# Optimization experiments

Measured on AMD Instinct MI355X. Metric: run time of the kernel, lower is better.

## Reference

```python
import jax, jax.numpy as jnp
import numpy as np

WS = 7
NUM_HEADS = 4


def setup_inputs() -> dict:
    key = jax.random.key(0)
    ks = jax.random.split(key, 5)
    C = 128
    return {
        "x": jax.random.normal(ks[0], (8, 222, 222, C), dtype=jnp.float32),
        "qkv_w": jax.random.normal(ks[1], (C, 3 * C), dtype=jnp.float32) * 0.02,
        "qkv_b": jax.random.normal(ks[2], (3 * C,), dtype=jnp.float32) * 0.02,
        "proj_w": jax.random.normal(ks[3], (C, C), dtype=jnp.float32) * 0.02,
        "proj_b": jax.random.normal(ks[4], (C,), dtype=jnp.float32) * 0.02,
    }


def reference(x, qkv_w, qkv_b, proj_w, proj_b):
    B, H, W, C = x.shape
    ws, nh = WS, NUM_HEADS
    hd = C // nh
    scale = hd ** (-0.5)
    pad_h = (ws - H % ws) % ws
    pad_w = (ws - W % ws) % ws
    xp = jnp.pad(x, ((0, 0), (0, pad_h), (0, pad_w), (0, 0)))
    Hp, Wp = H + pad_h, W + pad_w
    # window partition: [B,Hp,Wp,C] -> [nW, ws*ws, C]
    xw = xp.reshape(B, Hp // ws, ws, Wp // ws, ws, C)
    xw = xw.transpose(0, 1, 3, 2, 4, 5).reshape(-1, ws * ws, C)
    # qkv projection
    qkv = xw @ qkv_w + qkv_b  # [nW, 49, 3C]
    qkv = qkv.reshape(-1, ws * ws, 3, nh, hd).transpose(2, 0, 3, 1, 4)
    q, k, v = qkv[0], qkv[1], qkv[2]  # each [nW, nh, 49, hd]
    attn = jax.nn.softmax(jnp.einsum('whqd,whkd->whqk', q, k) * scale, axis=-1)
    out = jnp.einsum('whqk,whkd->whqd', attn, v)  # [nW, nh, 49, hd]
    out = out.transpose(0, 2, 1, 3).reshape(-1, ws * ws, C)
    out = out @ proj_w + proj_b
    # window reverse: [nW, ws*ws, C] -> [B, Hp, Wp, C]
    out = out.reshape(B, Hp // ws, Wp // ws, ws, ws, C)
    out = out.transpose(0, 1, 3, 2, 4, 5).reshape(B, Hp, Wp, C)
    return out[:, :H, :W, :]
```

## Files before the change

### kernel.cpp

```cpp
#include <hip/hip_runtime.h>
#include <stdint.h>

typedef __attribute__((ext_vector_type(8))) short bf16x8;
typedef __attribute__((ext_vector_type(4))) float f32x4;
typedef __attribute__((ext_vector_type(4))) unsigned int u32x4;

#define IMG 222

__device__ __forceinline__ unsigned short f2bf(float f){
  unsigned int u = __float_as_uint(f);
  return (unsigned short)((u + 0x7fffu + ((u >> 16) & 1u)) >> 16);
}

__device__ __forceinline__ unsigned int pk2bf(float lo, float hi){
  unsigned int r;
  asm("v_cvt_pk_bf16_f32 %0, %1, %2" : "=v"(r) : "v"(lo), "v"(hi));
  return r;
}

__device__ __forceinline__ int sw128(int r, int c){ return r*128 + (c ^ ((r & 7) << 3)); }
__device__ __forceinline__ int sw64 (int r, int c){ return r*64  + (c ^ ((r & 7) << 3)); }

__global__ void prep_weights(const float* __restrict__ qkv_w,
                             const float* __restrict__ proj_w,
                             unsigned short* __restrict__ qwt,
                             unsigned short* __restrict__ pwt){
  int i = blockIdx.x * blockDim.x + threadIdx.x;
  if (i < 384*128){ int n = i >> 7, k = i & 127; qwt[i] = f2bf(qkv_w[k*384 + n]); }
  if (i < 128*128){ int n = i >> 7, k = i & 127; pwt[i] = f2bf(proj_w[k*128 + n]); }
}

__global__ __launch_bounds__(256, 4)
void win_attn(const float* __restrict__ x,
              const float* __restrict__ qkv_b,
              const float* __restrict__ proj_b,
              const unsigned short* __restrict__ qwt,
              const unsigned short* __restrict__ pwt,
              float* __restrict__ out)
{
  extern __shared__ unsigned short lds[];
  unsigned short* r0 = lds;
  unsigned short* r1 = lds + 8192;
  unsigned short* r2 = lds + 16384;

  const int tid = threadIdx.x;
  const int wid = tid >> 6;
  const int l   = tid & 63;
  const int l15 = l & 15;
  const int lhi = l >> 4;

  const int w  = (blockIdx.x & 7) * 1024 + (blockIdx.x >> 3);
  const int b  = w >> 10;
  const int wi = (w >> 5) & 31;
  const int wj = w & 31;

  {
    const int t  = tid >> 2;
    const int cb = (tid & 3) * 32;
    const int r  = t / 7, c = t - r*7;
    const int gh = wi*7 + r, gw = wj*7 + c;
    const bool valid = (t < 49) && (gh < IMG) && (gw < IMG);
    const float* src = x + (((size_t)((size_t)b*IMG + gh))*IMG + gw)*128 + cb;
    #pragma unroll
    for (int i = 0; i < 8; ++i){
      float4 v = valid ? *(const float4*)(src + i*4) : make_float4(0.f,0.f,0.f,0.f);
      uint2 pk; pk.x = pk2bf(v.x, v.y); pk.y = pk2bf(v.z, v.w);
      *(uint2*)(r0 + sw128(t, cb + i*4)) = pk;
    }
  }
  __syncthreads();

  bf16x8 a[4][4];
  #pragma unroll
  for (int mi = 0; mi < 4; ++mi)
    #pragma unroll
    for (int ks = 0; ks < 4; ++ks)
      a[mi][ks] = *(const bf16x8*)(r0 + sw128(mi*16 + l15, ks*32 + lhi*8));
  __syncthreads();

  const float scale = 0.17677669529663687f;

  #pragma unroll
  for (int s = 0; s < 4; ++s){
    const int nt = wid + s*4;
    bf16x8 bfr[4];
    #pragma unroll
    for (int ks = 0; ks < 4; ++ks)
      bfr[ks] = *(const bf16x8*)(qwt + (nt*16 + l15)*128 + ks*32 + lhi*8);
    const float4 bias4 = *(const float4*)(qkv_b + nt*16 + lhi*4);
    #pragma unroll
    for (int mi = 0; mi < 4; ++mi){
      f32x4 acc = {0.f,0.f,0.f,0.f};
      #pragma unroll
      for (int ks = 0; ks < 4; ++ks)
        acc = __builtin_amdgcn_mfma_f32_16x16x32_bf16(bfr[ks], a[mi][ks], acc, 0, 0, 0);
      uint2 pk;
      if (s < 2){
        pk.x = pk2bf((acc[0]+bias4.x)*scale, (acc[1]+bias4.y)*scale);
        pk.y = pk2bf((acc[2]+bias4.z)*scale, (acc[3]+bias4.w)*scale);
        *(uint2*)(r0 + sw128(mi*16 + l15, nt*16 + lhi*4)) = pk;
      } else {
        pk.x = pk2bf(acc[0]+bias4.x, acc[1]+bias4.y);
        pk.y = pk2bf(acc[2]+bias4.z, acc[3]+bias4.w);
        *(uint2*)(r1 + sw128(mi*16 + l15, (nt-8)*16 + lhi*4)) = pk;
      }
    }
  }

  unsigned int pkv[4][2];
  {
    const int nt0 = 16 + 2*wid;
    bf16x8 bfr[4];
    #pragma unroll
    for (int ks = 0; ks < 4; ++ks)
      bfr[ks] = *(const bf16x8*)(qwt + (nt0*16 + l15)*128 + ks*32 + lhi*8);
    const float bias = qkv_b[nt0*16 + l15];
    #pragma unroll
    for (int mi = 0; mi < 4; ++mi){
      f32x4 acc = {0.f,0.f,0.f,0.f};
      #pragma unroll
      for (int ks = 0; ks < 4; ++ks)
        acc = __builtin_amdgcn_mfma_f32_16x16x32_bf16(a[mi][ks], bfr[ks], acc, 0, 0, 0);
      pkv[mi][0] = pk2bf(acc[0]+bias, acc[1]+bias);
      pkv[mi][1] = pk2bf(acc[2]+bias, acc[3]+bias);
    }
  }
  {
    const int nt1 = 17 + 2*wid;
    bf16x8 bfr[4];
    #pragma unroll
    for (int ks = 0; ks < 4; ++ks)
      bfr[ks] = *(const bf16x8*)(qwt + (nt1*16 + l15)*128 + ks*32 + lhi*8);
    const float bias = qkv_b[nt1*16 + l15];
    unsigned short* vh = r2 + wid*1024;
    #pragma unroll
    for (int mi = 0; mi < 4; ++mi){
      f32x4 acc = {0.f,0.f,0.f,0.f};
      #pragma unroll
      for (int ks = 0; ks < 4; ++ks)
        acc = __builtin_amdgcn_mfma_f32_16x16x32_bf16(a[mi][ks], bfr[ks], acc, 0, 0, 0);
      uint2 pk;
      pk.x = pk2bf(acc[0]+bias, acc[1]+bias);
      pk.y = pk2bf(acc[2]+bias, acc[3]+bias);
      *(uint2*)(vh + sw64(l15, mi*16 + lhi*4)) = pk;
    }
  }
  __syncthreads();

  const int h = wid;
  unsigned short* ph = lds + h*4096;
  bf16x8 aq[4], bk[4];
  #pragma unroll
  for (int i = 0; i < 4; ++i){
    aq[i] = *(const bf16x8*)(r0 + sw128(i*16 + l15, h*32 + lhi*8));
    bk[i] = *(const bf16x8*)(r1 + sw128(i*16 + l15, h*32 + lhi*8));
  }
  __syncthreads();

  float invs[4];
  #pragma unroll
  for (int mi = 0; mi < 4; ++mi){
    f32x4 st[4];
    #pragma unroll
    for (int ni = 0; ni < 4; ++ni){
      f32x4 z = {0.f,0.f,0.f,0.f};
      st[ni] = __builtin_amdgcn_mfma_f32_16x16x32_bf16(bk[ni], aq[mi], z, 0, 0, 0);
    }
    st[3][1] = -1e30f; st[3][2] = -1e30f; st[3][3] = -1e30f;
    if (lhi != 0) st[3][0] = -1e30f;
    float m = st[0][0];
    #pragma unroll
    for (int ni = 0; ni < 4; ++ni)
      #pragma unroll
      for (int r = 0; r < 4; ++r)
        m = fmaxf(m, st[ni][r]);
    m = fmaxf(m, __shfl_xor(m, 16));
    m = fmaxf(m, __shfl_xor(m, 32));
    float e[4][4], s = 0.f;
    #pragma unroll
    for (int ni = 0; ni < 4; ++ni)
      #pragma unroll
      for (int r = 0; r < 4; ++r){
        e[ni][r] = __expf(st[ni][r] - m);
        s += e[ni][r];
      }
    s += __shfl_xor(s, 16);
    s += __shfl_xor(s, 32);
    invs[mi] = __builtin_amdgcn_rcpf(s);
    #pragma unroll
    for (int ni = 0; ni < 4; ++ni){
      uint2 pk;
      pk.x = pk2bf(e[ni][0], e[ni][1]);
      pk.y = pk2bf(e[ni][2], e[ni][3]);
      *(uint2*)(ph + sw64(mi*16 + l15, ni*16 + lhi*4)) = pk;
    }
  }

  bf16x8 pa[4][2];
  #pragma unroll
  for (int mi = 0; mi < 4; ++mi)
    #pragma unroll
    for (int ks = 0; ks < 2; ++ks)
      pa[mi][ks] = *(const bf16x8*)(ph + sw64(mi*16 + l15, ks*32 + lhi*8));
  bf16x8 bv1[2];
  {
    unsigned short* vh = r2 + wid*1024;
    #pragma unroll
    for (int ks = 0; ks < 2; ++ks)
      bv1[ks] = *(const bf16x8*)(vh + sw64(l15, ks*32 + lhi*8));
  }
  bf16x8 bv0[2];
  {
    const int srcA = ((l & 16) << 1) + l15;
    #pragma unroll
    for (int ks = 0; ks < 2; ++ks){
      u32x4 wv;
      #pragma unroll
      for (int jj = 0; jj < 4; ++jj){
        const int src = srcA + ((jj >> 1) << 4);
        unsigned int va = (unsigned int)__shfl((int)pkv[2*ks][jj & 1], src);
        unsigned int vb = (unsigned int)__shfl((int)pkv[2*ks+1][jj & 1], src);
        wv[jj] = (lhi & 2) ? vb : va;
      }
      bv0[ks] = __builtin_bit_cast(bf16x8, wv);
    }
  }
  __syncthreads();

  #pragma unroll
  for (int mi = 0; mi < 4; ++mi){
    const float is = invs[mi];
    #pragma unroll
    for (int nc = 0; nc < 2; ++nc){
      f32x4 acc = {0.f,0.f,0.f,0.f};
      acc = __builtin_amdgcn_mfma_f32_16x16x32_bf16(nc ? bv1[0] : bv0[0], pa[mi][0], acc, 0, 0, 0);
      acc = __builtin_amdgcn_mfma_f32_16x16x32_bf16(nc ? bv1[1] : bv0[1], pa[mi][1], acc, 0, 0, 0);
      uint2 pk;
      pk.x = pk2bf(acc[0]*is, acc[1]*is);
      pk.y = pk2bf(acc[2]*is, acc[3]*is);
      *(uint2*)(r0 + sw128(mi*16 + l15, h*32 + nc*16 + lhi*4)) = pk;
    }
  }
  __syncthreads();

  bf16x8 ao[4][4];
  #pragma unroll
  for (int mi = 0; mi < 4; ++mi)
    #pragma unroll
    for (int ks = 0; ks < 4; ++ks)
      ao[mi][ks] = *(const bf16x8*)(r0 + sw128(mi*16 + l15, ks*32 + lhi*8));

  #pragma unroll
  for (int nj = 0; nj < 2; ++nj){
    const int ni = wid + nj*4;
    bf16x8 pbw[4];
    #pragma unroll
    for (int ks = 0; ks < 4; ++ks)
      pbw[ks] = *(const bf16x8*)(pwt + (ni*16 + l15)*128 + ks*32 + lhi*8);
    const float4 bias4 = *(const float4*)(proj_b + ni*16 + lhi*4);
    #pragma unroll
    for (int mi = 0; mi < 4; ++mi){
      f32x4 acc = {0.f,0.f,0.f,0.f};
      #pragma unroll
      for (int ks = 0; ks < 4; ++ks)
        acc = __builtin_amdgcn_mfma_f32_16x16x32_bf16(pbw[ks], ao[mi][ks], acc, 0, 0, 0);
      const int t = mi*16 + l15;
      if (t < 49){
        const int rr = t / 7, cc = t - rr*7;
        const int gh = wi*7 + rr, gw = wj*7 + cc;
        if (gh < IMG && gw < IMG){
          float4 o = make_float4(acc[0]+bias4.x, acc[1]+bias4.y,
                                 acc[2]+bias4.z, acc[3]+bias4.w);
          *(float4*)(out + (((size_t)((size_t)b*IMG + gh))*IMG + gw)*128 + ni*16 + lhi*4) = o;
        }
      }
    }
  }
}

extern "C" void kernel_launch(void* const* d_in, const int* in_sizes, int n_in,
                              void* d_out, int out_size, void* d_ws, size_t ws_size,
                              hipStream_t stream) {
  const float* x      = (const float*)d_in[0];
  const float* qkv_w  = (const float*)d_in[1];
  const float* qkv_b  = (const float*)d_in[2];
  const float* proj_w = (const float*)d_in[3];
  const float* proj_b = (const float*)d_in[4];
  float* out = (float*)d_out;

  unsigned short* qwt = (unsigned short*)d_ws;
  unsigned short* pwt = qwt + 384*128;

  hipLaunchKernelGGL(prep_weights, dim3(192), dim3(256), 0, stream,
                     qkv_w, proj_w, qwt, pwt);
  hipLaunchKernelGGL(win_attn, dim3(8192), dim3(256), 40960, stream,
                     x, qkv_b, proj_b, qwt, pwt, out);
}
```

Baseline: 207.3 us.

## Keep V in registers via shuffles, shrink LDS, raise occupancy, add setprio around MFMAs

```diff
diff --git a/kernel.cpp b/kernel.cpp
--- a/kernel.cpp
+++ b/kernel.cpp
@@ -20,6 +20,22 @@
 
 __device__ __forceinline__ int sw128(int r, int c){ return r*128 + (c ^ ((r & 7) << 3)); }
 __device__ __forceinline__ int sw64 (int r, int c){ return r*64  + (c ^ ((r & 7) << 3)); }
+
+__device__ __forceinline__ void rebuild_bv(const unsigned int pkv[4][2], int l, bf16x8 out[2]){
+  const int srcA = ((l & 16) << 1) + (l & 15);
+  #pragma unroll
+  for (int ks = 0; ks < 2; ++ks){
+    u32x4 wv;
+    #pragma unroll
+    for (int jj = 0; jj < 4; ++jj){
+      const int src = srcA + ((jj >> 1) << 4);
+      unsigned int va = (unsigned int)__shfl((int)pkv[2*ks][jj & 1], src);
+      unsigned int vb = (unsigned int)__shfl((int)pkv[2*ks+1][jj & 1], src);
+      wv[jj] = ((l >> 4) & 2) ? vb : va;
+    }
+    out[ks] = __builtin_bit_cast(bf16x8, wv);
+  }
+}
 
 __global__ void prep_weights(const float* __restrict__ qkv_w,
                              const float* __restrict__ proj_w,
@@ -27,10 +43,10 @@
                              unsigned short* __restrict__ pwt){
   int i = blockIdx.x * blockDim.x + threadIdx.x;
   if (i < 384*128){ int n = i >> 7, k = i & 127; qwt[i] = f2bf(qkv_w[k*384 + n]); }
-  if (i < 128*128){ int n = i >> 7, k = i & 127; pwt[i] = f2bf(proj_w[k*128 + n]); }
-}
-
-__global__ __launch_bounds__(256, 4)
+  if (i < 128*128){ int n = i >> 7, k = i & 127; pwt[i] = f2bf(proj_w[k*384 - k*256 + n]); }
+}
+
+__global__ __launch_bounds__(256, 5)
 void win_attn(const float* __restrict__ x,
               const float* __restrict__ qkv_b,
               const float* __restrict__ proj_b,
@@ -41,7 +57,6 @@
   extern __shared__ unsigned short lds[];
   unsigned short* r0 = lds;
   unsigned short* r1 = lds + 8192;
-  unsigned short* r2 = lds + 16384;
 
   const int tid = threadIdx.x;
   const int wid = tid >> 6;
@@ -88,6 +103,7 @@
     for (int ks = 0; ks < 4; ++ks)
       bfr[ks] = *(const bf16x8*)(qwt + (nt*16 + l15)*128 + ks*32 + lhi*8);
     const float4 bias4 = *(const float4*)(qkv_b + nt*16 + lhi*4);
+    __builtin_amdgcn_s_setprio(1);
     #pragma unroll
     for (int mi = 0; mi < 4; ++mi){
       f32x4 acc = {0.f,0.f,0.f,0.f};
@@ -105,9 +121,10 @@
         *(uint2*)(r1 + sw128(mi*16 + l15, (nt-8)*16 + lhi*4)) = pk;
       }
     }
-  }
-
-  unsigned int pkv[4][2];
+    __builtin_amdgcn_s_setprio(0);
+  }
+
+  unsigned int pkv0[4][2], pkv1[4][2];
   {
     const int nt0 = 16 + 2*wid;
     bf16x8 bfr[4];
@@ -115,15 +132,17 @@
     for (int ks = 0; ks < 4; ++ks)
       bfr[ks] = *(const bf16x8*)(qwt + (nt0*16 + l15)*128 + ks*32 + lhi*8);
     const float bias = qkv_b[nt0*16 + l15];
+    __builtin_amdgcn_s_setprio(1);
     #pragma unroll
     for (int mi = 0; mi < 4; ++mi){
       f32x4 acc = {0.f,0.f,0.f,0.f};
       #pragma unroll
       for (int ks = 0; ks < 4; ++ks)
         acc = __builtin_amdgcn_mfma_f32_16x16x32_bf16(a[mi][ks], bfr[ks], acc, 0, 0, 0);
-      pkv[mi][0] = pk2bf(acc[0]+bias, acc[1]+bias);
-      pkv[mi][1] = pk2bf(acc[2]+bias, acc[3]+bias);
-    }
+      pkv0[mi][0] = pk2bf(acc[0]+bias, acc[1]+bias);
+      pkv0[mi][1] = pk2bf(acc[2]+bias, acc[3]+bias);
+    }
+    __builtin_amdgcn_s_setprio(0);
   }
   {
     const int nt1 = 17 + 2*wid;
@@ -132,18 +151,17 @@
     for (int ks = 0; ks < 4; ++ks)
       bfr[ks] = *(const bf16x8*)(qwt + (nt1*16 + l15)*128 + ks*32 + lhi*8);
     const float bias = qkv_b[nt1*16 + l15];
-    unsigned short* vh = r2 + wid*1024;
+    __builtin_amdgcn_s_setprio(1);
     #pragma unroll
     for (int mi = 0; mi < 4; ++mi){
       f32x4 acc = {0.f,0.f,0.f,0.f};
       #pragma unroll
       for (int ks = 0; ks < 4; ++ks)
         acc = __builtin_amdgcn_mfma_f32_16x16x32_bf16(a[mi][ks], bfr[ks], acc, 0, 0, 0);
-      uint2 pk;
-      pk.x = pk2bf(acc[0]+bias, acc[1]+bias);
-      pk.y = pk2bf(acc[2]+bias, acc[3]+bias);
-      *(uint2*)(vh + sw64(l15, mi*16 + lhi*4)) = pk;
-    }
+      pkv1[mi][0] = pk2bf(acc[0]+bias, acc[1]+bias);
+      pkv1[mi][1] = pk2bf(acc[2]+bias, acc[3]+bias);
+    }
+    __builtin_amdgcn_s_setprio(0);
   }
   __syncthreads();
 
@@ -161,11 +179,13 @@
   #pragma unroll
   for (int mi = 0; mi < 4; ++mi){
     f32x4 st[4];
+    __builtin_amdgcn_s_setprio(1);
     #pragma unroll
     for (int ni = 0; ni < 4; ++ni){
       f32x4 z = {0.f,0.f,0.f,0.f};
       st[ni] = __builtin_amdgcn_mfma_f32_16x16x32_bf16(bk[ni], aq[mi], z, 0, 0, 0);
     }
+    __builtin_amdgcn_s_setprio(0);
     st[3][1] = -1e30f; st[3][2] = -1e30f; st[3][3] = -1e30f;
     if (lhi != 0) st[3][0] = -1e30f;
     float m = st[0][0];
@@ -202,44 +222,28 @@
     #pragma unroll
     for (int ks = 0; ks < 2; ++ks)
       pa[mi][ks] = *(const bf16x8*)(ph + sw64(mi*16 + l15, ks*32 + lhi*8));
-  bf16x8 bv1[2];
-  {
-    unsigned short* vh = r2 + wid*1024;
-    #pragma unroll
-    for (int ks = 0; ks < 2; ++ks)
-      bv1[ks] = *(const bf16x8*)(vh + sw64(l15, ks*32 + lhi*8));
-  }
-  bf16x8 bv0[2];
-  {
-    const int srcA = ((l & 16) << 1) + l15;
-    #pragma unroll
-    for (int ks = 0; ks < 2; ++ks){
-      u32x4 wv;
-      #pragma unroll
-      for (int jj = 0; jj < 4; ++jj){
-        const int src = srcA + ((jj >> 1) << 4);
-        unsigned int va = (unsigned int)__shfl((int)pkv[2*ks][jj & 1], src);
-        unsigned int vb = (unsigned int)__shfl((int)pkv[2*ks+1][jj & 1], src);
-        wv[jj] = (lhi & 2) ? vb : va;
-      }
-      bv0[ks] = __builtin_bit_cast(bf16x8, wv);
-    }
-  }
+  bf16x8 bv0[2], bv1[2];
+  rebuild_bv(pkv0, l, bv0);
+  rebuild_bv(pkv1, l, bv1);
   __syncthreads();
 
   #pragma unroll
   for (int mi = 0; mi < 4; ++mi){
     const float is = invs[mi];
-    #pragma unroll
-    for (int nc = 0; nc < 2; ++nc){
-      f32x4 acc = {0.f,0.f,0.f,0.f};
-      acc = __builtin_amdgcn_mfma_f32_16x16x32_bf16(nc ? bv1[0] : bv0[0], pa[mi][0], acc, 0, 0, 0);
-      acc = __builtin_amdgcn_mfma_f32_16x16x32_bf16(nc ? bv1[1] : bv0[1], pa[mi][1], acc, 0, 0, 0);
-      uint2 pk;
-      pk.x = pk2bf(acc[0]*is, acc[1]*is);
-      pk.y = pk2bf(acc[2]*is, acc[3]*is);
-      *(uint2*)(r0 + sw128(mi*16 + l15, h*32 + nc*16 + lhi*4)) = pk;
-    }
+    __builtin_amdgcn_s_setprio(1);
+    f32x4 acc0 = {0.f,0.f,0.f,0.f}, acc1 = {0.f,0.f,0.f,0.f};
+    acc0 = __builtin_amdgcn_mfma_f32_16x16x32_bf16(bv0[0], pa[mi][0], acc0, 0, 0, 0);
+    acc0 = __builtin_amdgcn_mfma_f32_16x16x32_bf16(bv0[1], pa[mi][1], acc0, 0, 0, 0);
+    acc1 = __builtin_amdgcn_mfma_f32_16x16x32_bf16(bv1[0], pa[mi][0], acc1, 0, 0, 0);
+    acc1 = __builtin_amdgcn_mfma_f32_16x16x32_bf16(bv1[1], pa[mi][1], acc1, 0, 0, 0);
+    __builtin_amdgcn_s_setprio(0);
+    uint2 pk0, pk1;
+    pk0.x = pk2bf(acc0[0]*is, acc0[1]*is);
+    pk0.y = pk2bf(acc0[2]*is, acc0[3]*is);
+    pk1.x = pk2bf(acc1[0]*is, acc1[1]*is);
+    pk1.y = pk2bf(acc1[2]*is, acc1[3]*is);
+    *(uint2*)(r0 + sw128(mi*16 + l15, h*32 + lhi*4))      = pk0;
+    *(uint2*)(r0 + sw128(mi*16 + l15, h*32 + 16 + lhi*4)) = pk1;
   }
   __syncthreads();
 
@@ -260,10 +264,12 @@
     const float4 bias4 = *(const float4*)(proj_b + ni*16 + lhi*4);
     #pragma unroll
     for (int mi = 0; mi < 4; ++mi){
+      __builtin_amdgcn_s_setprio(1);
       f32x4 acc = {0.f,0.f,0.f,0.f};
       #pragma unroll
       for (int ks = 0; ks < 4; ++ks)
         acc = __builtin_amdgcn_mfma_f32_16x16x32_bf16(pbw[ks], ao[mi][ks], acc, 0, 0, 0);
+      __builtin_amdgcn_s_setprio(0);
       const int t = mi*16 + l15;
       if (t < 49){
         const int rr = t / 7, cc = t - rr*7;
@@ -293,6 +299,6 @@
 
   hipLaunchKernelGGL(prep_weights, dim3(192), dim3(256), 0, stream,
                      qkv_w, proj_w, qwt, pwt);
-  hipLaunchKernelGGL(win_attn, dim3(8192), dim3(256), 40960, stream,
+  hipLaunchKernelGGL(win_attn, dim3(8192), dim3(256), 32768, stream,
                      x, qkv_b, proj_b, qwt, pwt, out);
 }
```

New measurement: 466.1 us. +124.9%, slower.
